# Kernel optimization log

Measured on AMD Instinct MI355X. Metric: run time of the kernel, lower is better.

The kernel has to match this reference:

```python
import jax, jax.numpy as jnp
import numpy as np

D, DFF, H, NLAYERS, B, L, U = 1536, 2048, 8, 2, 16, 64, 64
EPS = 1e-5


def _ln(x, w, b):
    mu = jnp.mean(x, axis=-1, keepdims=True)
    var = jnp.mean((x - mu) ** 2, axis=-1, keepdims=True)
    return (x - mu) / jnp.sqrt(var + EPS) * w + b


def _mha(q_in, kv_in, qkv_w, qkv_b, out_w, out_b, mask):
    # torch nn.MultiheadAttention: packed in_proj [3D,D], out_proj [D,D]
    d = q_in.shape[-1]
    hd = d // H
    wq, wk, wv = jnp.split(qkv_w, 3, axis=0)
    bq, bk, bv = jnp.split(qkv_b, 3, axis=0)
    q = q_in @ wq.T + bq
    k = kv_in @ wk.T + bk
    v = kv_in @ wv.T + bv
    def heads(t):
        b_, s_, _ = t.shape
        return t.reshape(b_, s_, H, hd).transpose(0, 2, 1, 3)  # [B,H,S,hd]
    q, k, v = heads(q), heads(k), heads(v)
    scores = jnp.einsum('bhqd,bhkd->bhqk', q, k) / jnp.sqrt(jnp.float32(hd))
    if mask is not None:
        scores = scores + mask  # [Sq,Sk] broadcast
    attn = jax.nn.softmax(scores, axis=-1)
    o = jnp.einsum('bhqk,bhkd->bhqd', attn, v)
    b_, _, s_, _ = o.shape
    o = o.transpose(0, 2, 1, 3).reshape(b_, s_, d)
    return o @ out_w.T + out_b


def setup_inputs() -> dict:
    key = jax.random.key(0)
    ks = jax.random.split(key, 16)
    f = lambda k, shp: (jax.random.normal(k, shp, jnp.float32) * 0.02)
    Lyr = NLAYERS
    return {
        'x': jax.random.normal(ks[0], (B, L, U, D), jnp.float32),
        'pooler_w': f(ks[1], (1, D)),
        'pooler_b': jnp.zeros((1,), jnp.float32),
        'pos_embed': f(ks[2], (1, 128, D)),
        'sa_qkv_w': f(ks[3], (Lyr, 3 * D, D)),
        'sa_qkv_b': jnp.zeros((Lyr, 3 * D), jnp.float32),
        'sa_out_w': f(ks[4], (Lyr, D, D)),
        'sa_out_b': jnp.zeros((Lyr, D), jnp.float32),
        'ca_qkv_w': f(ks[5], (Lyr, 3 * D, D)),
        'ca_qkv_b': jnp.zeros((Lyr, 3 * D), jnp.float32),
        'ca_out_w': f(ks[6], (Lyr, D, D)),
        'ca_out_b': jnp.zeros((Lyr, D), jnp.float32),
        'ff1_w': f(ks[7], (Lyr, DFF, D)),
        'ff1_b': jnp.zeros((Lyr, DFF), jnp.float32),
        'ff2_w': f(ks[8], (Lyr, D, DFF)),
        'ff2_b': jnp.zeros((Lyr, D), jnp.float32),
        'ln1_w': jnp.ones((Lyr, D), jnp.float32),
        'ln1_b': jnp.zeros((Lyr, D), jnp.float32),
        'ln2_w': jnp.ones((Lyr, D), jnp.float32),
        'ln2_b': jnp.zeros((Lyr, D), jnp.float32),
        'ln3_w': jnp.ones((Lyr, D), jnp.float32),
        'ln3_b': jnp.zeros((Lyr, D), jnp.float32),
    }


def reference(x, pooler_w, pooler_b, pos_embed,
              sa_qkv_w, sa_qkv_b, sa_out_w, sa_out_b,
              ca_qkv_w, ca_qkv_b, ca_out_w, ca_out_b,
              ff1_w, ff1_b, ff2_w, ff2_b,
              ln1_w, ln1_b, ln2_w, ln2_b, ln3_w, ln3_b):
    b, l, u, d = x.shape
    # SelfAttentionPooling over utterance tokens (vectorized over dialogue dim)
    logits = jnp.einsum('blud,d->blu', x, pooler_w[0]) + pooler_b[0]
    att = jax.nn.softmax(logits, axis=-1)
    pooled = jnp.einsum('blu,blud->bld', att, x)

    pos = pos_embed[:, :l, :]
    memory = pooled + pos
    tgt = pooled + pos
    causal = jnp.triu(jnp.full((l, l), -jnp.inf, jnp.float32), 1)

    h = tgt
    for i in range(NLAYERS):
        # post-norm TransformerDecoderLayer (torch default norm_first=False)
        h = _ln(h + _mha(h, h, sa_qkv_w[i], sa_qkv_b[i], sa_out_w[i], sa_out_b[i], causal),
                ln1_w[i], ln1_b[i])
        h = _ln(h + _mha(h, memory, ca_qkv_w[i], ca_qkv_b[i], ca_out_w[i], ca_out_b[i], None),
                ln2_w[i], ln2_b[i])
        ff = jax.nn.relu(h @ ff1_w[i].T + ff1_b[i]) @ ff2_w[i].T + ff2_b[i]
        h = _ln(h + ff, ln3_w[i], ln3_b[i])

    # loop over prefixes t=1..L-1 taking the last position == causal positions 0..L-2
    return h[:, : l - 1, :]
```

## Files before the change

kernel.cpp:

```cpp
#include <hip/hip_runtime.h>
#include <math.h>

#define D_MODEL 1536
#define NH      8
#define HD      192
#define BB      16
#define LL      64
#define UU      64
#define NTOK    1024
#define EPSF    1e-5f

typedef __bf16 bf16;
typedef __bf16 bf16x4_t __attribute__((ext_vector_type(4)));
typedef __bf16 bf16x8_t __attribute__((ext_vector_type(8)));
typedef float  f32x4_t  __attribute__((ext_vector_type(4)));

__device__ __forceinline__ void gload_lds16(const bf16* g, bf16* l) {
    __builtin_amdgcn_global_load_lds((const __attribute__((address_space(1))) void*)g,
                                     (__attribute__((address_space(3))) void*)l, 16, 0, 0);
}

__global__ __launch_bounds__(256)
void cvt_all_kernel(const float* __restrict__ s0, const float* __restrict__ s1,
                    const float* __restrict__ s2, const float* __restrict__ s3,
                    const float* __restrict__ s4, const float* __restrict__ s5,
                    bf16* __restrict__ dst)
{
    const int c0 = 3538944, c1 = 4718592, c2 = 8257536,
              c3 = 9437184, c4 = 11010048, c5 = 12582912;
    for (int i = blockIdx.x * 256 + threadIdx.x; i < c5; i += gridDim.x * 256) {
        const float* s; int j;
        if      (i < c0) { s = s0; j = i; }
        else if (i < c1) { s = s1; j = i - c0; }
        else if (i < c2) { s = s2; j = i - c1; }
        else if (i < c3) { s = s3; j = i - c2; }
        else if (i < c4) { s = s4; j = i - c3; }
        else             { s = s5; j = i - c4; }
        const float4 v = ((const float4*)s)[j];
        bf16x4_t o = { (bf16)v.x, (bf16)v.y, (bf16)v.z, (bf16)v.w };
        ((bf16x4_t*)dst)[i] = o;
    }
}

__global__ __launch_bounds__(256)
void fusedpool_kernel(const float* __restrict__ x, const float* __restrict__ pw,
                      const float* __restrict__ pb, const float* __restrict__ pos,
                      float* __restrict__ h, bf16* __restrict__ hb,
                      bf16* __restrict__ memb)
{
    __shared__ float red[2][4];
    const int t = threadIdx.x, wave = t >> 6, lane = t & 63;
    const int bl = blockIdx.x, l = bl & (LL - 1);
    const float* xb = x + (size_t)bl * UU * D_MODEL;

    float pwr[6];
#pragma unroll
    for (int j = 0; j < 6; ++j) pwr[j] = pw[t + j * 256];
    const float pb0 = pb[0];

    float xv[2][6];
#pragma unroll
    for (int j = 0; j < 6; ++j) xv[0][j] = xb[t + j * 256];

    float m = -__builtin_inff(), den = 0.f;
    float acc[6] = {0.f, 0.f, 0.f, 0.f, 0.f, 0.f};

    for (int u = 0; u < UU; ++u) {
        const int cur = u & 1;
        if (u < UU - 1) {
            const float* xn = xb + (size_t)(u + 1) * D_MODEL;
#pragma unroll
            for (int j = 0; j < 6; ++j) xv[cur ^ 1][j] = xn[t + j * 256];
        }
        float p = 0.f;
#pragma unroll
        for (int j = 0; j < 6; ++j) p += xv[cur][j] * pwr[j];
#pragma unroll
        for (int off = 32; off; off >>= 1) p += __shfl_xor(p, off, 64);
        if (lane == 0) red[cur][wave] = p;
        __syncthreads();
        const float logit = red[cur][0] + red[cur][1] + red[cur][2] + red[cur][3] + pb0;
        const float nm = fmaxf(m, logit);
        const float sc = __expf(m - nm);
        const float w  = __expf(logit - nm);
#pragma unroll
        for (int j = 0; j < 6; ++j) acc[j] = acc[j] * sc + w * xv[cur][j];
        den = den * sc + w;
        m = nm;
    }

    const float inv = 1.f / den;
    const size_t db = (size_t)bl * D_MODEL;
    const int pp = l * D_MODEL;
#pragma unroll
    for (int j = 0; j < 6; ++j) {
        const int d = t + j * 256;
        const float v = acc[j] * inv + pos[pp + d];
        h[db + d] = v;
        hb[db + d] = (bf16)v;
        memb[db + d] = (bf16)v;
    }
}

template<int MODE, bool DUAL>
__global__ __launch_bounds__(512, 4)
void gemm8_kernel(const bf16* __restrict__ A, const bf16* __restrict__ W,
                  const float* __restrict__ bias, void* __restrict__ Cv,
                  int N, int K, int split,
                  const bf16* __restrict__ A2, const bf16* __restrict__ W2,
                  const float* __restrict__ bias2, void* __restrict__ Cv2, int N2)
{
    __shared__ bf16 As[2][64 * 64];
    __shared__ bf16 Bs[2][128 * 64];
    const int t = threadIdx.x, wave = t >> 6, lane = t & 63;

    const int T = gridDim.x, fid = blockIdx.x;
    int vid = (fid & 7) * (T >> 3) + (fid >> 3);
    const bf16* Ap = A; const bf16* Wp = W; const float* bp = bias;
    void* Cp = Cv; int Nn = N;
    if (DUAL && vid >= split) { vid -= split; Ap = A2; Wp = W2; bp = bias2; Cp = Cv2; Nn = N2; }
    const int m0 = (vid & 15) * 64;
    const int n0 = (vid >> 4) * 128;

    const int wm = wave >> 2, wn = wave & 3;
    const int frow = lane & 15, kq = lane >> 4, s = frow & 7;
    const int lr = lane >> 3;
    const int g8 = ((lane & 7) ^ lr) * 8;

    f32x4_t acc[2][2] = {};

    const bf16* Abase = Ap + (size_t)(m0 + wave * 8 + lr) * K + g8;
    const bf16* Wbase = Wp + (size_t)(n0 + wave * 8 + lr) * K + g8;

    gload_lds16(Abase, &As[0][wave * 512]);
    gload_lds16(Wbase, &Bs[0][wave * 512]);
    gload_lds16(Wbase + (size_t)64 * K, &Bs[0][4096 + wave * 512]);
    __syncthreads();

    const int nt = K >> 6;
    int cur = 0;
    for (int tt = 0; tt < nt; ++tt) {
        if (tt + 1 < nt) {
            const int k0 = (tt + 1) << 6;
            gload_lds16(Abase + k0, &As[cur ^ 1][wave * 512]);
            gload_lds16(Wbase + k0, &Bs[cur ^ 1][wave * 512]);
            gload_lds16(Wbase + k0 + (size_t)64 * K, &Bs[cur ^ 1][4096 + wave * 512]);
        }
#pragma unroll
        for (int kk = 0; kk < 2; ++kk) {
            const int gg = (((kk << 2) | kq) ^ s) * 8;
            bf16x8_t af[2], bv[2];
#pragma unroll
            for (int mi = 0; mi < 2; ++mi)
                af[mi] = *(const bf16x8_t*)&As[cur][(wm * 32 + mi * 16 + frow) * 64 + gg];
#pragma unroll
            for (int ni = 0; ni < 2; ++ni)
                bv[ni] = *(const bf16x8_t*)&Bs[cur][(wn * 32 + ni * 16 + frow) * 64 + gg];
#pragma unroll
            for (int mi = 0; mi < 2; ++mi)
#pragma unroll
                for (int ni = 0; ni < 2; ++ni)
                    acc[mi][ni] = __builtin_amdgcn_mfma_f32_16x16x32_bf16(af[mi], bv[ni], acc[mi][ni], 0, 0, 0);
        }
        __syncthreads();
        cur ^= 1;
    }

    const int crow = m0 + wm * 32 + kq * 4;
    const int ccol = n0 + wn * 32 + frow;
#pragma unroll
    for (int mi = 0; mi < 2; ++mi)
#pragma unroll
        for (int ni = 0; ni < 2; ++ni) {
            const int col = ccol + ni * 16;
            const float bvv = bp[col];
            const int rb = crow + mi * 16;
#pragma unroll
            for (int j = 0; j < 4; ++j) {
                float v = acc[mi][ni][j] + bvv;
                if (MODE == 0) {
                    ((float*)Cp)[(size_t)(rb + j) * Nn + col] = v;
                } else {
                    ((bf16*)Cp)[(size_t)(rb + j) * Nn + col] = (bf16)fmaxf(v, 0.f);
                }
            }
        }
}

template<bool CAUSAL>
__global__ __launch_bounds__(256)
void attn_kernel(const float* __restrict__ qbuf, int qstride, int qoff0,
                 const float* __restrict__ kbuf, int kstride, int koff0,
                 const float* __restrict__ vbuf, int vstride, int voff0,
                 bf16* __restrict__ out)
{
    __shared__ float kv[HD * 64];
    __shared__ float sc[16 * 64];
    const int t = threadIdx.x, wave = t >> 6, lane = t & 63;
    const int bh = blockIdx.x >> 2, qh = blockIdx.x & 3;
    const int b = bh >> 3, hh = bh & 7;
    const int t0 = b * 64;
    const float scale = rsqrtf((float)HD);

    for (int i = 0; i < 48; ++i) {
        const int idx = t + i * 256;
        const int r = idx / HD, c = idx % HD;
        kv[c * 64 + (r ^ (c & 31))] = kbuf[(size_t)(t0 + r) * kstride + koff0 + hh * HD + c];
    }
    __syncthreads();

    for (int qi = 0; qi < 4; ++qi) {
        const int ql = wave * 4 + qi;
        const int q = qh * 16 + ql;
        const float* qr = qbuf + (size_t)(t0 + q) * qstride + qoff0 + hh * HD;
        float a = 0.f;
#pragma unroll 8
        for (int d = 0; d < HD; ++d)
            a += qr[d] * kv[d * 64 + (lane ^ (d & 31))];
        a *= scale;
        if (CAUSAL && lane > q) a = -__builtin_inff();
        float m = a;
#pragma unroll
        for (int off = 32; off; off >>= 1) m = fmaxf(m, __shfl_xor(m, off, 64));
        float e = (CAUSAL && lane > q) ? 0.f : __expf(a - m);
        float s = e;
#pragma unroll
        for (int off = 32; off; off >>= 1) s += __shfl_xor(s, off, 64);
        sc[ql * 64 + lane] = e / s;
    }
    __syncthreads();

    for (int i = 0; i < 48; ++i) {
        const int idx = t + i * 256;
        const int r = idx / HD, c = idx % HD;
        kv[r * HD + c] = vbuf[(size_t)(t0 + r) * vstride + voff0 + hh * HD + c];
    }
    __syncthreads();

    for (int qi = 0; qi < 4; ++qi) {
        const int ql = wave * 4 + qi;
        const int q = qh * 16 + ql;
        float o0 = 0.f, o1 = 0.f, o2 = 0.f;
#pragma unroll 8
        for (int k = 0; k < 64; ++k) {
            const float p = sc[ql * 64 + k];
            o0 += p * kv[k * HD + lane];
            o1 += p * kv[k * HD + 64 + lane];
            o2 += p * kv[k * HD + 128 + lane];
        }
        bf16* op = out + (size_t)(t0 + q) * D_MODEL + hh * HD;
        op[lane] = (bf16)o0; op[64 + lane] = (bf16)o1; op[128 + lane] = (bf16)o2;
    }
}

__global__ __launch_bounds__(256)
void ln_kernel(const float* __restrict__ a, const float* __restrict__ r,
               const float* __restrict__ w, const float* __restrict__ bb,
               float* __restrict__ out, bf16* __restrict__ outb)
{
    __shared__ float red[8];
    const int tok = blockIdx.x, t = threadIdx.x;
    const int wave = t >> 6, lane = t & 63;
    const float* ap = a + (size_t)tok * D_MODEL;
    const float* rp = r + (size_t)tok * D_MODEL;
    float v[6];
    float s = 0.f;
#pragma unroll
    for (int j = 0; j < 6; ++j) { v[j] = ap[t + j * 256] + rp[t + j * 256]; s += v[j]; }
#pragma unroll
    for (int off = 32; off; off >>= 1) s += __shfl_xor(s, off, 64);
    if (lane == 0) red[wave] = s;
    __syncthreads();
    const float mu = (red[0] + red[1] + red[2] + red[3]) * (1.f / D_MODEL);
    float s2 = 0.f;
#pragma unroll
    for (int j = 0; j < 6; ++j) { const float d = v[j] - mu; s2 += d * d; }
#pragma unroll
    for (int off = 32; off; off >>= 1) s2 += __shfl_xor(s2, off, 64);
    if (lane == 0) red[4 + wave] = s2;
    __syncthreads();
    const float var = (red[4] + red[5] + red[6] + red[7]) * (1.f / D_MODEL);
    const float inv = rsqrtf(var + EPSF);
#pragma unroll
    for (int j = 0; j < 6; ++j) {
        const int d = t + j * 256;
        const float o = (v[j] - mu) * inv * w[d] + bb[d];
        out[(size_t)tok * D_MODEL + d] = o;
        outb[(size_t)tok * D_MODEL + d] = (bf16)o;
    }
}

__global__ __launch_bounds__(256)
void slice_kernel(const float* __restrict__ h, float* __restrict__ out)
{
    const int i = blockIdx.x * 256 + threadIdx.x;
    if (i >= BB * 63 * (D_MODEL / 4)) return;
    const int d4 = i % (D_MODEL / 4);
    const int tl = i / (D_MODEL / 4);
    const int b = tl / 63, l = tl % 63;
    ((float4*)out)[i] = ((const float4*)(h + (size_t)(b * 64 + l) * D_MODEL))[d4];
}

extern "C" void kernel_launch(void* const* d_in, const int* in_sizes, int n_in,
                              void* d_out, int out_size, void* d_ws, size_t ws_size,
                              hipStream_t stream)
{
    (void)in_sizes; (void)n_in; (void)out_size; (void)ws_size;
    const float* x        = (const float*)d_in[0];
    const float* pooler_w = (const float*)d_in[1];
    const float* pooler_b = (const float*)d_in[2];
    const float* pos      = (const float*)d_in[3];
    const float* sa_qkv_w = (const float*)d_in[4];
    const float* sa_qkv_b = (const float*)d_in[5];
    const float* sa_out_w = (const float*)d_in[6];
    const float* sa_out_b = (const float*)d_in[7];
    const float* ca_qkv_w = (const float*)d_in[8];
    const float* ca_qkv_b = (const float*)d_in[9];
    const float* ca_out_w = (const float*)d_in[10];
    const float* ca_out_b = (const float*)d_in[11];
    const float* ff1_w    = (const float*)d_in[12];
    const float* ff1_b    = (const float*)d_in[13];
    const float* ff2_w    = (const float*)d_in[14];
    const float* ff2_b    = (const float*)d_in[15];
    const float* ln1_w    = (const float*)d_in[16];
    const float* ln1_b    = (const float*)d_in[17];
    const float* ln2_w    = (const float*)d_in[18];
    const float* ln2_b    = (const float*)d_in[19];
    const float* ln3_w    = (const float*)d_in[20];
    const float* ln3_b    = (const float*)d_in[21];
    float* outp = (float*)d_out;

    char* ws = (char*)d_ws;
    size_t off = 0;
    auto alloc = [&](size_t bytes) { char* p = ws + off; off += (bytes + 255) & ~(size_t)255; return p; };

    const size_t E_QKV = (size_t)4608 * D_MODEL;
    const size_t E_SQ  = (size_t)D_MODEL * D_MODEL;
    const size_t E_F1  = (size_t)2048 * D_MODEL;

    bf16* wb_sa_qkv = (bf16*)alloc(2 * E_QKV * 2);
    bf16* wb_sa_out = (bf16*)alloc(2 * E_SQ * 2);
    bf16* wb_ca_qkv = (bf16*)alloc(2 * E_QKV * 2);
    bf16* wb_ca_out = (bf16*)alloc(2 * E_SQ * 2);
    bf16* wb_ff1    = (bf16*)alloc(2 * E_F1 * 2);
    bf16* wb_ff2    = (bf16*)alloc(2 * E_F1 * 2);
    float* h     = (float*)alloc((size_t)NTOK * D_MODEL * 4);
    bf16*  hb    = (bf16*) alloc((size_t)NTOK * D_MODEL * 2);
    bf16*  memb  = (bf16*) alloc((size_t)NTOK * D_MODEL * 2);
    float* qkv   = (float*)alloc((size_t)NTOK * 4608 * 4);
    float* cq    = (float*)alloc((size_t)NTOK * D_MODEL * 4);
    float* ckv0  = (float*)alloc((size_t)NTOK * 3072 * 4);
    float* ckv1  = (float*)alloc((size_t)NTOK * 3072 * 4);
    bf16*  attno = (bf16*) alloc((size_t)NTOK * D_MODEL * 2);
    float* proj  = (float*)alloc((size_t)NTOK * D_MODEL * 4);
    bf16*  ffmid = (bf16*) alloc((size_t)NTOK * 2048 * 2);

    cvt_all_kernel<<<2048, 256, 0, stream>>>(sa_qkv_w, sa_out_w, ca_qkv_w,
                                             ca_out_w, ff1_w, ff2_w, wb_sa_qkv);
    fusedpool_kernel<<<NTOK, 256, 0, stream>>>(x, pooler_w, pooler_b, pos, h, hb, memb);

    gemm8_kernel<0, true><<<768, 512, 0, stream>>>(
        memb, wb_ca_qkv + (size_t)1536 * D_MODEL, ca_qkv_b + 1536,
        ckv0, 3072, D_MODEL, 384,
        memb, wb_ca_qkv + E_QKV + (size_t)1536 * D_MODEL, ca_qkv_b + 4608 + 1536,
        ckv1, 3072);

    for (int i = 0; i < 2; ++i) {
        float* ckv = i ? ckv1 : ckv0;

        gemm8_kernel<0, false><<<16 * 36, 512, 0, stream>>>(
            hb, wb_sa_qkv + (size_t)i * E_QKV, sa_qkv_b + (size_t)i * 4608,
            qkv, 4608, D_MODEL, 0, nullptr, nullptr, nullptr, nullptr, 0);
        attn_kernel<true><<<BB * NH * 4, 256, 0, stream>>>(
            qkv, 4608, 0, qkv, 4608, 1536, qkv, 4608, 3072, attno);
        gemm8_kernel<0, false><<<16 * 12, 512, 0, stream>>>(
            attno, wb_sa_out + (size_t)i * E_SQ, sa_out_b + (size_t)i * D_MODEL,
            proj, D_MODEL, D_MODEL, 0, nullptr, nullptr, nullptr, nullptr, 0);
        ln_kernel<<<NTOK, 256, 0, stream>>>(h, proj, ln1_w + i * D_MODEL, ln1_b + i * D_MODEL, h, hb);

        gemm8_kernel<0, false><<<16 * 12, 512, 0, stream>>>(
            hb, wb_ca_qkv + (size_t)i * E_QKV, ca_qkv_b + (size_t)i * 4608,
            cq, D_MODEL, D_MODEL, 0, nullptr, nullptr, nullptr, nullptr, 0);
        attn_kernel<false><<<BB * NH * 4, 256, 0, stream>>>(
            cq, 1536, 0, ckv, 3072, 0, ckv, 3072, 1536, attno);
        gemm8_kernel<0, false><<<16 * 12, 512, 0, stream>>>(
            attno, wb_ca_out + (size_t)i * E_SQ, ca_out_b + (size_t)i * D_MODEL,
            proj, D_MODEL, D_MODEL, 0, nullptr, nullptr, nullptr, nullptr, 0);
        ln_kernel<<<NTOK, 256, 0, stream>>>(h, proj, ln2_w + i * D_MODEL, ln2_b + i * D_MODEL, h, hb);

        gemm8_kernel<1, false><<<16 * 16, 512, 0, stream>>>(
            hb, wb_ff1 + (size_t)i * E_F1, ff1_b + (size_t)i * 2048,
            ffmid, 2048, D_MODEL, 0, nullptr, nullptr, nullptr, nullptr, 0);
        gemm8_kernel<0, false><<<16 * 12, 512, 0, stream>>>(
            ffmid, wb_ff2 + (size_t)i * E_F1, ff2_b + (size_t)i * D_MODEL,
            proj, D_MODEL, 2048, 0, nullptr, nullptr, nullptr, nullptr, 0);
        ln_kernel<<<NTOK, 256, 0, stream>>>(h, proj, ln3_w + i * D_MODEL, ln3_b + i * D_MODEL, h, hb);
    }

    slice_kernel<<<(BB * 63 * (D_MODEL / 4) + 255) / 256, 256, 0, stream>>>(h, outp);
}
```

Measured before the change: 773.8 us.

## Use split-K for small GEMMs and fuse partial reductions into consumers

Adds a split-K=2 mode to the bf16 GEMM kernel, doubling the grid for the out-projection, cross-attention query, FF1 and FF2 GEMMs. The two fp32 partials are summed inside layernorm, inside the cross-attention query load, or by a new reduce+ReLU kernel for FF1. The final output slice is folded into the last layernorm, removing a separate kernel. The aim is better CU occupancy for GEMMs with few tiles, at the cost of extra partial-buffer traffic.

```diff
diff --git a/kernel.cpp b/kernel.cpp
--- a/kernel.cpp
+++ b/kernel.cpp
@@ -102,7 +102,7 @@
     }
 }
 
-template<int MODE, bool DUAL>
+template<int MODE, bool DUAL, bool SPLITK>
 __global__ __launch_bounds__(512, 4)
 void gemm8_kernel(const bf16* __restrict__ A, const bf16* __restrict__ W,
                   const float* __restrict__ bias, void* __restrict__ Cv,
@@ -119,8 +119,11 @@
     const bf16* Ap = A; const bf16* Wp = W; const float* bp = bias;
     void* Cp = Cv; int Nn = N;
     if (DUAL && vid >= split) { vid -= split; Ap = A2; Wp = W2; bp = bias2; Cp = Cv2; Nn = N2; }
+    int kslice = 0;
+    if (SPLITK) { kslice = vid & 1; vid >>= 1; }
     const int m0 = (vid & 15) * 64;
     const int n0 = (vid >> 4) * 128;
+    const int kbase = SPLITK ? kslice * (K >> 1) : 0;
 
     const int wm = wave >> 2, wn = wave & 3;
     const int frow = lane & 15, kq = lane >> 4, s = frow & 7;
@@ -129,15 +132,15 @@
 
     f32x4_t acc[2][2] = {};
 
-    const bf16* Abase = Ap + (size_t)(m0 + wave * 8 + lr) * K + g8;
-    const bf16* Wbase = Wp + (size_t)(n0 + wave * 8 + lr) * K + g8;
+    const bf16* Abase = Ap + (size_t)(m0 + wave * 8 + lr) * K + kbase + g8;
+    const bf16* Wbase = Wp + (size_t)(n0 + wave * 8 + lr) * K + kbase + g8;
 
     gload_lds16(Abase, &As[0][wave * 512]);
     gload_lds16(Wbase, &Bs[0][wave * 512]);
     gload_lds16(Wbase + (size_t)64 * K, &Bs[0][4096 + wave * 512]);
     __syncthreads();
 
-    const int nt = K >> 6;
+    const int nt = SPLITK ? (K >> 7) : (K >> 6);
     int cur = 0;
     for (int tt = 0; tt < nt; ++tt) {
         if (tt + 1 < nt) {
@@ -166,6 +169,7 @@
         cur ^= 1;
     }
 
+    float* Cpart = (float*)Cp + (SPLITK ? (size_t)kslice * NTOK * Nn : 0);
     const int crow = m0 + wm * 32 + kq * 4;
     const int ccol = n0 + wn * 32 + frow;
 #pragma unroll
@@ -173,13 +177,13 @@
 #pragma unroll
         for (int ni = 0; ni < 2; ++ni) {
             const int col = ccol + ni * 16;
-            const float bvv = bp[col];
+            const float bvv = (SPLITK && kslice) ? 0.f : bp[col];
             const int rb = crow + mi * 16;
 #pragma unroll
             for (int j = 0; j < 4; ++j) {
                 float v = acc[mi][ni][j] + bvv;
                 if (MODE == 0) {
-                    ((float*)Cp)[(size_t)(rb + j) * Nn + col] = v;
+                    Cpart[(size_t)(rb + j) * Nn + col] = v;
                 } else {
                     ((bf16*)Cp)[(size_t)(rb + j) * Nn + col] = (bf16)fmaxf(v, 0.f);
                 }
@@ -187,9 +191,23 @@
         }
 }
 
-template<bool CAUSAL>
 __global__ __launch_bounds__(256)
-void attn_kernel(const float* __restrict__ qbuf, int qstride, int qoff0,
+void reduce_relu_kernel(const float* __restrict__ p0, const float* __restrict__ p1,
+                        bf16* __restrict__ dst, int n4)
+{
+    const int i = blockIdx.x * 256 + threadIdx.x;
+    if (i >= n4) return;
+    const float4 a = ((const float4*)p0)[i];
+    const float4 b = ((const float4*)p1)[i];
+    bf16x4_t o = { (bf16)fmaxf(a.x + b.x, 0.f), (bf16)fmaxf(a.y + b.y, 0.f),
+                   (bf16)fmaxf(a.z + b.z, 0.f), (bf16)fmaxf(a.w + b.w, 0.f) };
+    ((bf16x4_t*)dst)[i] = o;
+}
+
+template<bool CAUSAL, bool QSPLIT>
+__global__ __launch_bounds__(256)
+void attn_kernel(const float* __restrict__ qbuf, const float* __restrict__ qbuf2,
+                 int qstride, int qoff0,
                  const float* __restrict__ kbuf, int kstride, int koff0,
                  const float* __restrict__ vbuf, int vstride, int voff0,
                  bf16* __restrict__ out)
@@ -212,11 +230,15 @@
     for (int qi = 0; qi < 4; ++qi) {
         const int ql = wave * 4 + qi;
         const int q = qh * 16 + ql;
-        const float* qr = qbuf + (size_t)(t0 + q) * qstride + qoff0 + hh * HD;
+        const size_t qb0 = (size_t)(t0 + q) * qstride + qoff0 + hh * HD;
+        const float* qr  = qbuf + qb0;
+        const float* qr2 = QSPLIT ? (qbuf2 + qb0) : nullptr;
         float a = 0.f;
 #pragma unroll 8
-        for (int d = 0; d < HD; ++d)
-            a += qr[d] * kv[d * 64 + (lane ^ (d & 31))];
+        for (int d = 0; d < HD; ++d) {
+            const float qv = QSPLIT ? (qr[d] + qr2[d]) : qr[d];
+            a += qv * kv[d * 64 + (lane ^ (d & 31))];
+        }
         a *= scale;
         if (CAUSAL && lane > q) a = -__builtin_inff();
         float m = a;
@@ -253,20 +275,28 @@
     }
 }
 
+template<bool R2, bool SLICE>
 __global__ __launch_bounds__(256)
 void ln_kernel(const float* __restrict__ a, const float* __restrict__ r,
+               const float* __restrict__ r2,
                const float* __restrict__ w, const float* __restrict__ bb,
-               float* __restrict__ out, bf16* __restrict__ outb)
+               float* __restrict__ out, bf16* __restrict__ outb,
+               float* __restrict__ out2)
 {
     __shared__ float red[8];
     const int tok = blockIdx.x, t = threadIdx.x;
     const int wave = t >> 6, lane = t & 63;
     const float* ap = a + (size_t)tok * D_MODEL;
     const float* rp = r + (size_t)tok * D_MODEL;
+    const float* rp2 = R2 ? (r2 + (size_t)tok * D_MODEL) : nullptr;
     float v[6];
     float s = 0.f;
 #pragma unroll
-    for (int j = 0; j < 6; ++j) { v[j] = ap[t + j * 256] + rp[t + j * 256]; s += v[j]; }
+    for (int j = 0; j < 6; ++j) {
+        v[j] = ap[t + j * 256] + rp[t + j * 256];
+        if (R2) v[j] += rp2[t + j * 256];
+        s += v[j];
+    }
 #pragma unroll
     for (int off = 32; off; off >>= 1) s += __shfl_xor(s, off, 64);
     if (lane == 0) red[wave] = s;
@@ -281,24 +311,15 @@
     __syncthreads();
     const float var = (red[4] + red[5] + red[6] + red[7]) * (1.f / D_MODEL);
     const float inv = rsqrtf(var + EPSF);
+    const int bq = tok >> 6, lq = tok & 63;
 #pragma unroll
     for (int j = 0; j < 6; ++j) {
         const int d = t + j * 256;
         const float o = (v[j] - mu) * inv * w[d] + bb[d];
         out[(size_t)tok * D_MODEL + d] = o;
         outb[(size_t)tok * D_MODEL + d] = (bf16)o;
-    }
-}
-
-__global__ __launch_bounds__(256)
-void slice_kernel(const float* __restrict__ h, float* __restrict__ out)
-{
-    const int i = blockIdx.x * 256 + threadIdx.x;
-    if (i >= BB * 63 * (D_MODEL / 4)) return;
-    const int d4 = i % (D_MODEL / 4);
-    const int tl = i / (D_MODEL / 4);
-    const int b = tl / 63, l = tl % 63;
-    ((float4*)out)[i] = ((const float4*)(h + (size_t)(b * 64 + l) * D_MODEL))[d4];
+        if (SLICE && lq < 63) out2[(size_t)(bq * 63 + lq) * D_MODEL + d] = o;
+    }
 }
 
 extern "C" void kernel_launch(void* const* d_in, const int* in_sizes, int n_in,
@@ -348,18 +369,23 @@
     bf16*  hb    = (bf16*) alloc((size_t)NTOK * D_MODEL * 2);
     bf16*  memb  = (bf16*) alloc((size_t)NTOK * D_MODEL * 2);
     float* qkv   = (float*)alloc((size_t)NTOK * 4608 * 4);
-    float* cq    = (float*)alloc((size_t)NTOK * D_MODEL * 4);
+    float* cq01  = (float*)alloc((size_t)NTOK * D_MODEL * 4 * 2);
     float* ckv0  = (float*)alloc((size_t)NTOK * 3072 * 4);
     float* ckv1  = (float*)alloc((size_t)NTOK * 3072 * 4);
     bf16*  attno = (bf16*) alloc((size_t)NTOK * D_MODEL * 2);
-    float* proj  = (float*)alloc((size_t)NTOK * D_MODEL * 4);
+    float* proj01= (float*)alloc((size_t)NTOK * D_MODEL * 4 * 2);
+    float* f1p01 = (float*)alloc((size_t)NTOK * 2048 * 4 * 2);
     bf16*  ffmid = (bf16*) alloc((size_t)NTOK * 2048 * 2);
+
+    float* proj1 = proj01 + (size_t)NTOK * D_MODEL;
+    float* cq1   = cq01   + (size_t)NTOK * D_MODEL;
+    float* f1p1  = f1p01  + (size_t)NTOK * 2048;
 
     cvt_all_kernel<<<2048, 256, 0, stream>>>(sa_qkv_w, sa_out_w, ca_qkv_w,
                                              ca_out_w, ff1_w, ff2_w, wb_sa_qkv);
     fusedpool_kernel<<<NTOK, 256, 0, stream>>>(x, pooler_w, pooler_b, pos, h, hb, memb);
 
-    gemm8_kernel<0, true><<<768, 512, 0, stream>>>(
+    gemm8_kernel<0, true, false><<<768, 512, 0, stream>>>(
         memb, wb_ca_qkv + (size_t)1536 * D_MODEL, ca_qkv_b + 1536,
         ckv0, 3072, D_MODEL, 384,
         memb, wb_ca_qkv + E_QKV + (size_t)1536 * D_MODEL, ca_qkv_b + 4608 + 1536,
@@ -368,34 +394,41 @@
     for (int i = 0; i < 2; ++i) {
         float* ckv = i ? ckv1 : ckv0;
 
-        gemm8_kernel<0, false><<<16 * 36, 512, 0, stream>>>(
+        gemm8_kernel<0, false, false><<<16 * 36, 512, 0, stream>>>(
             hb, wb_sa_qkv + (size_t)i * E_QKV, sa_qkv_b + (size_t)i * 4608,
             qkv, 4608, D_MODEL, 0, nullptr, nullptr, nullptr, nullptr, 0);
-        attn_kernel<true><<<BB * NH * 4, 256, 0, stream>>>(
-            qkv, 4608, 0, qkv, 4608, 1536, qkv, 4608, 3072, attno);
-        gemm8_kernel<0, false><<<16 * 12, 512, 0, stream>>>(
+        attn_kernel<true, false><<<BB * NH * 4, 256, 0, stream>>>(
+            qkv, nullptr, 4608, 0, qkv, 4608, 1536, qkv, 4608, 3072, attno);
+        gemm8_kernel<0, false, true><<<16 * 12 * 2, 512, 0, stream>>>(
             attno, wb_sa_out + (size_t)i * E_SQ, sa_out_b + (size_t)i * D_MODEL,
-            proj, D_MODEL, D_MODEL, 0, nullptr, nullptr, nullptr, nullptr, 0);
-        ln_kernel<<<NTOK, 256, 0, stream>>>(h, proj, ln1_w + i * D_MODEL, ln1_b + i * D_MODEL, h, hb);
-
-        gemm8_kernel<0, false><<<16 * 12, 512, 0, stream>>>(
+            proj01, D_MODEL, D_MODEL, 0, nullptr, nullptr, nullptr, nullptr, 0);
+        ln_kernel<true, false><<<NTOK, 256, 0, stream>>>(
+            h, proj01, proj1, ln1_w + i * D_MODEL, ln1_b + i * D_MODEL, h, hb, nullptr);
+
+        gemm8_kernel<0, false, true><<<16 * 12 * 2, 512, 0, stream>>>(
             hb, wb_ca_qkv + (size_t)i * E_QKV, ca_qkv_b + (size_t)i * 4608,
-            cq, D_MODEL, D_MODEL, 0, nullptr, nullptr, nullptr, nullptr, 0);
-        attn_kernel<false><<<BB * NH * 4, 256, 0, stream>>>(
-            cq, 1536, 0, ckv, 3072, 0, ckv, 3072, 1536, attno);
-        gemm8_kernel<0, false><<<16 * 12, 512, 0, stream>>>(
+            cq01, D_MODEL, D_MODEL, 0, nullptr, nullptr, nullptr, nullptr, 0);
+        attn_kernel<false, true><<<BB * NH * 4, 256, 0, stream>>>(
+            cq01, cq1, 1536, 0, ckv, 3072, 0, ckv, 3072, 1536, attno);
+        gemm8_kernel<0, false, true><<<16 * 12 * 2, 512, 0, stream>>>(
             attno, wb_ca_out + (size_t)i * E_SQ, ca_out_b + (size_t)i * D_MODEL,
-            proj, D_MODEL, D_MODEL, 0, nullptr, nullptr, nullptr, nullptr, 0);
-        ln_kernel<<<NTOK, 256, 0, stream>>>(h, proj, ln2_w + i * D_MODEL, ln2_b + i * D_MODEL, h, hb);
-
-        gemm8_kernel<1, false><<<16 * 16, 512, 0, stream>>>(
+            proj01, D_MODEL, D_MODEL, 0, nullptr, nullptr, nullptr, nullptr, 0);
+        ln_kernel<true, false><<<NTOK, 256, 0, stream>>>(
+            h, proj01, proj1, ln2_w + i * D_MODEL, ln2_b + i * D_MODEL, h, hb, nullptr);
+
+        gemm8_kernel<0, false, true><<<16 * 16 * 2, 512, 0, stream>>>(
             hb, wb_ff1 + (size_t)i * E_F1, ff1_b + (size_t)i * 2048,
-            ffmid, 2048, D_MODEL, 0, nullptr, nullptr, nullptr, nullptr, 0);
-        gemm8_kernel<0, false><<<16 * 12, 512, 0, stream>>>(
+            f1p01, 2048, D_MODEL, 0, nullptr, nullptr, nullptr, nullptr, 0);
+        reduce_relu_kernel<<<2048, 256, 0, stream>>>(
+            f1p01, f1p1, ffmid, NTOK * 2048 / 4);
+        gemm8_kernel<0, false, true><<<16 * 12 * 2, 512, 0, stream>>>(
             ffmid, wb_ff2 + (size_t)i * E_F1, ff2_b + (size_t)i * D_MODEL,
-            proj, D_MODEL, 2048, 0, nullptr, nullptr, nullptr, nullptr, 0);
-        ln_kernel<<<NTOK, 256, 0, stream>>>(h, proj, ln3_w + i * D_MODEL, ln3_b + i * D_MODEL, h, hb);
-    }
-
-    slice_kernel<<<(BB * 63 * (D_MODEL / 4) + 255) / 256, 256, 0, stream>>>(h, outp);
-}
+            proj01, D_MODEL, 2048, 0, nullptr, nullptr, nullptr, nullptr, 0);
+        if (i == 0)
+            ln_kernel<true, false><<<NTOK, 256, 0, stream>>>(
+                h, proj01, proj1, ln3_w, ln3_b, h, hb, nullptr);
+        else
+            ln_kernel<true, true><<<NTOK, 256, 0, stream>>>(
+                h, proj01, proj1, ln3_w + D_MODEL, ln3_b + D_MODEL, h, hb, outp);
+    }
+}
```

After: 695.3 us. -10.1%, faster.
